# Optimization experiments

Hardware: AMD Instinct MI355X
Metric: run time of the kernel (lower is better)

## Reference

```python
import jax, jax.numpy as jnp
import numpy as np

B, D, N = 65536, 512, 1024  # batch, latent_dim, som_dim**2


def setup_inputs() -> dict:
    key = jax.random.key(0)
    k1, k2, k3, k4, k5 = jax.random.split(key, 5)
    return {
        "x": jax.random.normal(k1, (B, D), dtype=jnp.float32),
        "W": jax.random.normal(k2, (D, D), dtype=jnp.float32) * 0.02,
        "b": jax.random.normal(k3, (D,), dtype=jnp.float32) * 0.02,
        "prototypes": jax.random.normal(k4, (N, D), dtype=jnp.float32),
        "temp_raw": jnp.array([0.5], dtype=jnp.float32),
    }


def reference(x, W, b, prototypes, temp_raw):
    # encoder_fc: Linear(latent_dim, latent_dim)
    z = x @ W.T + b  # [B, D]
    # torch.cdist (p=2) via ||z||^2 + ||p||^2 - 2 z.p, avoids [B,N,D] intermediate
    z_sq = jnp.sum(z * z, axis=-1, keepdims=True)          # [B, 1]
    p_sq = jnp.sum(prototypes * prototypes, axis=-1)        # [N]
    d2 = jnp.maximum(z_sq + p_sq - 2.0 * (z @ prototypes.T), 1e-12)
    dists = jnp.sqrt(d2)                                    # [B, N]
    # temperature = sigmoid(temp_raw) * (1 - 0.001) + 0.001
    temp = jax.nn.sigmoid(temp_raw[0]) * (1.0 - 0.001) + 0.001
    weights = jax.nn.softmax(-dists / temp, axis=-1)        # [B, N]
    blended = weights @ prototypes                          # [B, D]
    return blended, weights
```

## Files before the change

kernel.cpp:

```cpp
#include <hip/hip_runtime.h>

#define DDIM 512
#define NPROT 1024

typedef float fvec4 __attribute__((ext_vector_type(4)));
typedef __bf16 bf16x8 __attribute__((ext_vector_type(8)));
typedef unsigned short us4 __attribute__((ext_vector_type(4)));
typedef unsigned short us8 __attribute__((ext_vector_type(8)));
typedef __attribute__((address_space(1))) unsigned int gu32;
typedef __attribute__((address_space(3))) unsigned int lu32;

__device__ __forceinline__ unsigned short f2bf(float f) {
  unsigned u = __float_as_uint(f);
  u += 0x7fffu + ((u >> 16) & 1u);
  return (unsigned short)(u >> 16);
}
__device__ __forceinline__ float bf2f(unsigned short h) {
  return __uint_as_float(((unsigned)h) << 16);
}
__device__ __forceinline__ void gl_lds16(const void* g, void* l) {
  __builtin_amdgcn_global_load_lds((gu32*)(unsigned long long)g,
                                   (lu32*)(unsigned)(unsigned long long)l,
                                   16, 0, 0);
}

__global__ __launch_bounds__(256) void prep_kernel(
    const float* __restrict__ W, const float* __restrict__ P,
    unsigned short* __restrict__ Wb, unsigned short* __restrict__ Pb,
    unsigned short* __restrict__ PTb, float* __restrict__ psq) {
  __shared__ float tile[32][33];
  const int b = blockIdx.x;
  const int t = threadIdx.x;
  if (b < 256) {
    int e = (b * 256 + t) * 4;
    fvec4 v = *(const fvec4*)(W + e);
    us4 o; o.x = f2bf(v.x); o.y = f2bf(v.y); o.z = f2bf(v.z); o.w = f2bf(v.w);
    *(us4*)(Wb + e) = o;
  } else if (b < 768) {
    int e = ((b - 256) * 256 + t) * 4;
    fvec4 v = *(const fvec4*)(P + e);
    us4 o; o.x = f2bf(v.x); o.y = f2bf(v.y); o.z = f2bf(v.z); o.w = f2bf(v.w);
    *(us4*)(Pb + e) = o;
  } else if (b < 1280) {
    int rel = b - 768;
    int d0 = (rel >> 5) * 32;
    int n0 = (rel & 31) * 32;
    int r = t >> 3;
    int c4 = (t & 7) * 4;
    fvec4 v = *(const fvec4*)(P + (size_t)(n0 + r) * DDIM + d0 + c4);
    tile[r][c4 + 0] = v.x; tile[r][c4 + 1] = v.y;
    tile[r][c4 + 2] = v.z; tile[r][c4 + 3] = v.w;
    __syncthreads();
    us4 o;
    o.x = f2bf(tile[c4 + 0][r]);
    o.y = f2bf(tile[c4 + 1][r]);
    o.z = f2bf(tile[c4 + 2][r]);
    o.w = f2bf(tile[c4 + 3][r]);
    *(us4*)(PTb + (size_t)(d0 + r) * NPROT + n0 + c4) = o;
  } else {
    int l = t & 63;
    int row = (b - 1280) * 4 + (t >> 6);
    const float* pr = P + (size_t)row * DDIM;
    fvec4 a = *(const fvec4*)(pr + l * 4);
    fvec4 c = *(const fvec4*)(pr + 256 + l * 4);
    float s = a.x * a.x + a.y * a.y + a.z * a.z + a.w * a.w +
              c.x * c.x + c.y * c.y + c.z * c.z + c.w * c.w;
    for (int o = 32; o > 0; o >>= 1) s += __shfl_xor(s, o);
    if (l == 0) psq[row] = s;
  }
}

__global__ __launch_bounds__(256) void g1_kernel(
    const float* __restrict__ x, const unsigned short* __restrict__ Wb,
    const float* __restrict__ bias, unsigned short* __restrict__ z) {
  __shared__ unsigned short Ab[128 * 32];
  __shared__ unsigned short Bb[128 * 32];
  const int t = threadIdx.x;
  const int bi = blockIdx.x;
  const int bm = bi >> 2, bn = bi & 3;
  const int w = t >> 6, l = t & 63, lr = l & 15, lq = l >> 4;
  const int wm = (w >> 1) * 64, wn = (w & 1) * 64;
  fvec4 acc[4][4];
#pragma unroll
  for (int r = 0; r < 4; r++)
#pragma unroll
    for (int c = 0; c < 4; c++) acc[r][c] = 0.0f;
  const float* Ag = x + (size_t)bm * 128 * DDIM;
  const unsigned short* Bg = Wb + (size_t)bn * 128 * DDIM;
  for (int k0 = 0; k0 < DDIM; k0 += 32) {
    __syncthreads();
#pragma unroll
    for (int i = 0; i < 2; i++) {
      int c = i * 256 + t;
      gl_lds16(Bg + (size_t)(c >> 2) * DDIM + k0 + (c & 3) * 8, Bb + c * 8);
    }
#pragma unroll
    for (int i = 0; i < 4; i++) {
      int c = i * 256 + t;
      int row = c >> 3, j = (c & 7) * 4;
      fvec4 v = *(const fvec4*)(Ag + (size_t)row * DDIM + k0 + j);
      us4 o; o.x = f2bf(v.x); o.y = f2bf(v.y); o.z = f2bf(v.z); o.w = f2bf(v.w);
      *(us4*)(Ab + row * 32 + j) = o;
    }
    __syncthreads();
    bf16x8 af[4], bfr[4];
#pragma unroll
    for (int r = 0; r < 4; r++)
      af[r] = *(const bf16x8*)(Ab + (wm + r * 16 + lr) * 32 + lq * 8);
#pragma unroll
    for (int c = 0; c < 4; c++)
      bfr[c] = *(const bf16x8*)(Bb + (wn + c * 16 + lr) * 32 + lq * 8);
#pragma unroll
    for (int r = 0; r < 4; r++)
#pragma unroll
      for (int c = 0; c < 4; c++)
        acc[r][c] = __builtin_amdgcn_mfma_f32_16x16x32_bf16(af[r], bfr[c], acc[r][c], 0, 0, 0);
  }
  const int rbase = bm * 128 + wm + lq * 4;
  const int cbase = bn * 128 + wn + lr;
#pragma unroll
  for (int c = 0; c < 4; c++) {
    int col = cbase + c * 16;
    float bc = bias[col];
#pragma unroll
    for (int r = 0; r < 4; r++) {
      int row = rbase + r * 16;
#pragma unroll
      for (int v = 0; v < 4; v++)
        z[(size_t)(row + v) * DDIM + col] = f2bf(acc[r][c][v] + bc);
    }
  }
}

__global__ __launch_bounds__(256) void zsq_kernel(
    const unsigned short* __restrict__ z, float* __restrict__ zsq) {
  const int t = threadIdx.x, l = t & 63;
  const size_t row = (size_t)blockIdx.x * 4 + (t >> 6);
  us8 u = *(const us8*)(z + row * DDIM + l * 8);
  float s = 0.f;
#pragma unroll
  for (int i = 0; i < 8; i++) { float f = bf2f(u[i]); s += f * f; }
  for (int o = 32; o > 0; o >>= 1) s += __shfl_xor(s, o);
  if (l == 0) zsq[row] = s;
}

__global__ __launch_bounds__(256) void g2_kernel(
    const unsigned short* __restrict__ z, const unsigned short* __restrict__ Pb,
    const float* __restrict__ zsq, const float* __restrict__ psq,
    const float* __restrict__ temp_raw, float* __restrict__ logits) {
  __shared__ unsigned short Ab[128 * 32];
  __shared__ unsigned short Bb[128 * 32];
  const int t = threadIdx.x;
  const int bi = blockIdx.x;
  const int bm = bi >> 3, bn = bi & 7;
  const int w = t >> 6, l = t & 63, lr = l & 15, lq = l >> 4;
  const int wm = (w >> 1) * 64, wn = (w & 1) * 64;
  fvec4 acc[4][4];
#pragma unroll
  for (int r = 0; r < 4; r++)
#pragma unroll
    for (int c = 0; c < 4; c++) acc[r][c] = 0.0f;
  const unsigned short* Ag = z + (size_t)bm * 128 * DDIM;
  const unsigned short* Bg = Pb + (size_t)bn * 128 * DDIM;
  for (int k0 = 0; k0 < DDIM; k0 += 32) {
    __syncthreads();
#pragma unroll
    for (int i = 0; i < 2; i++) {
      int c = i * 256 + t;
      gl_lds16(Ag + (size_t)(c >> 2) * DDIM + k0 + (c & 3) * 8, Ab + c * 8);
      gl_lds16(Bg + (size_t)(c >> 2) * DDIM + k0 + (c & 3) * 8, Bb + c * 8);
    }
    __syncthreads();
    bf16x8 af[4], bfr[4];
#pragma unroll
    for (int r = 0; r < 4; r++)
      af[r] = *(const bf16x8*)(Ab + (wm + r * 16 + lr) * 32 + lq * 8);
#pragma unroll
    for (int c = 0; c < 4; c++)
      bfr[c] = *(const bf16x8*)(Bb + (wn + c * 16 + lr) * 32 + lq * 8);
#pragma unroll
    for (int r = 0; r < 4; r++)
#pragma unroll
      for (int c = 0; c < 4; c++)
        acc[r][c] = __builtin_amdgcn_mfma_f32_16x16x32_bf16(af[r], bfr[c], acc[r][c], 0, 0, 0);
  }
  const float temp = 0.999f / (1.0f + __expf(-temp_raw[0])) + 0.001f;
  const float nit = -1.0f / temp;
  const int rbase = bm * 128 + wm + lq * 4;
  const int cbase = bn * 128 + wn + lr;
  float zr[4][4];
#pragma unroll
  for (int r = 0; r < 4; r++)
#pragma unroll
    for (int v = 0; v < 4; v++) zr[r][v] = zsq[rbase + r * 16 + v];
#pragma unroll
  for (int c = 0; c < 4; c++) {
    int col = cbase + c * 16;
    float pc = psq[col];
#pragma unroll
    for (int r = 0; r < 4; r++)
#pragma unroll
      for (int v = 0; v < 4; v++) {
        float d2 = fmaxf(zr[r][v] + pc - 2.0f * acc[r][c][v], 1e-12f);
        logits[(size_t)(rbase + r * 16 + v) * NPROT + col] = nit * sqrtf(d2);
      }
  }
}

__global__ __launch_bounds__(256) void softmax_kernel(float* __restrict__ wio) {
  const int t = threadIdx.x, l = t & 63;
  float* p = wio + ((size_t)blockIdx.x * 4 + (t >> 6)) * NPROT;
  fvec4 v[4];
#pragma unroll
  for (int j = 0; j < 4; j++) v[j] = *(const fvec4*)(p + (j * 64 + l) * 4);
  float m = -3.4e38f;
#pragma unroll
  for (int j = 0; j < 4; j++)
    m = fmaxf(m, fmaxf(fmaxf(v[j].x, v[j].y), fmaxf(v[j].z, v[j].w)));
  for (int o = 32; o > 0; o >>= 1) m = fmaxf(m, __shfl_xor(m, o));
  float s = 0.f;
#pragma unroll
  for (int j = 0; j < 4; j++) {
    v[j].x = __expf(v[j].x - m); v[j].y = __expf(v[j].y - m);
    v[j].z = __expf(v[j].z - m); v[j].w = __expf(v[j].w - m);
    s += v[j].x + v[j].y + v[j].z + v[j].w;
  }
  for (int o = 32; o > 0; o >>= 1) s += __shfl_xor(s, o);
  const float rinv = 1.0f / s;
#pragma unroll
  for (int j = 0; j < 4; j++) {
    v[j] *= rinv;
    *(fvec4*)(p + (j * 64 + l) * 4) = v[j];
  }
}

__global__ __launch_bounds__(512) void g3_kernel(
    const float* __restrict__ wgt, const unsigned short* __restrict__ PTb,
    float* __restrict__ blended) {
  __shared__ unsigned short Ab[128 * 32];
  __shared__ unsigned short Bb[512 * 32];
  const int t = threadIdx.x;
  const int bm = blockIdx.x;
  const int w = t >> 6, l = t & 63, lr = l & 15, lq = l >> 4;
  const int wm = (w >> 2) * 64;
  const int wn = (w & 3) * 128;
  fvec4 acc[4][8];
#pragma unroll
  for (int r = 0; r < 4; r++)
#pragma unroll
    for (int c = 0; c < 8; c++) acc[r][c] = 0.0f;
  const float* Ag = wgt + (size_t)bm * 128 * NPROT;
  for (int k0 = 0; k0 < NPROT; k0 += 32) {
    __syncthreads();
#pragma unroll
    for (int i = 0; i < 4; i++) {
      int c = i * 512 + t;
      gl_lds16(PTb + (size_t)(c >> 2) * NPROT + k0 + (c & 3) * 8, Bb + c * 8);
    }
    {
      int row = t >> 2, j = (t & 3) * 8;
      const float* src = Ag + (size_t)row * NPROT + k0 + j;
      fvec4 v0 = *(const fvec4*)(src);
      fvec4 v1 = *(const fvec4*)(src + 4);
      us8 o;
      o[0] = f2bf(v0.x); o[1] = f2bf(v0.y); o[2] = f2bf(v0.z); o[3] = f2bf(v0.w);
      o[4] = f2bf(v1.x); o[5] = f2bf(v1.y); o[6] = f2bf(v1.z); o[7] = f2bf(v1.w);
      *(us8*)(Ab + row * 32 + j) = o;
    }
    __syncthreads();
    bf16x8 af[4], bfr[8];
#pragma unroll
    for (int r = 0; r < 4; r++)
      af[r] = *(const bf16x8*)(Ab + (wm + r * 16 + lr) * 32 + lq * 8);
#pragma unroll
    for (int c = 0; c < 8; c++)
      bfr[c] = *(const bf16x8*)(Bb + (wn + c * 16 + lr) * 32 + lq * 8);
#pragma unroll
    for (int r = 0; r < 4; r++)
#pragma unroll
      for (int c = 0; c < 8; c++)
        acc[r][c] = __builtin_amdgcn_mfma_f32_16x16x32_bf16(af[r], bfr[c], acc[r][c], 0, 0, 0);
  }
  const int rbase = bm * 128 + wm + lq * 4;
#pragma unroll
  for (int c = 0; c < 8; c++) {
    int col = wn + c * 16 + lr;
#pragma unroll
    for (int r = 0; r < 4; r++) {
      int row = rbase + r * 16;
#pragma unroll
      for (int v = 0; v < 4; v++)
        blended[(size_t)(row + v) * DDIM + col] = acc[r][c][v];
    }
  }
}

extern "C" void kernel_launch(void* const* d_in, const int* in_sizes, int n_in,
                              void* d_out, int out_size, void* d_ws, size_t ws_size,
                              hipStream_t stream) {
  (void)in_sizes; (void)n_in; (void)out_size; (void)ws_size;
  const float* x  = (const float*)d_in[0];
  const float* W  = (const float*)d_in[1];
  const float* bv = (const float*)d_in[2];
  const float* P  = (const float*)d_in[3];
  const float* tr = (const float*)d_in[4];

  float* out = (float*)d_out;
  float* blended = out;
  float* weights = out + (size_t)65536 * DDIM;
  unsigned short* zbuf = (unsigned short*)d_out;

  char* ws = (char*)d_ws;
  unsigned short* Wb  = (unsigned short*)(ws + 0);
  unsigned short* Pb  = (unsigned short*)(ws + 524288);
  unsigned short* PTb = (unsigned short*)(ws + 1572864);
  float* psq = (float*)(ws + 2621440);
  float* zsq = (float*)(ws + 2625536);

  prep_kernel<<<dim3(1536), 256, 0, stream>>>(W, P, Wb, Pb, PTb, psq);
  g1_kernel<<<dim3(2048), 256, 0, stream>>>(x, Wb, bv, zbuf);
  zsq_kernel<<<dim3(16384), 256, 0, stream>>>(zbuf, zsq);
  g2_kernel<<<dim3(4096), 256, 0, stream>>>(zbuf, Pb, zsq, psq, tr, weights);
  softmax_kernel<<<dim3(16384), 256, 0, stream>>>(weights);
  g3_kernel<<<dim3(512), 512, 0, stream>>>(weights, PTb, blended);
}
```

Baseline: 908.2 us.

## Fuse zsq into GEMM1 epilogue and softmax into GEMM2/GEMM3 via row-sum atomics

```diff
diff --git a/kernel.cpp b/kernel.cpp
--- a/kernel.cpp
+++ b/kernel.cpp
@@ -27,7 +27,8 @@
 __global__ __launch_bounds__(256) void prep_kernel(
     const float* __restrict__ W, const float* __restrict__ P,
     unsigned short* __restrict__ Wb, unsigned short* __restrict__ Pb,
-    unsigned short* __restrict__ PTb, float* __restrict__ psq) {
+    unsigned short* __restrict__ PTb, float* __restrict__ psq,
+    float* __restrict__ zsq) {
   __shared__ float tile[32][33];
   const int b = blockIdx.x;
   const int t = threadIdx.x;
@@ -57,7 +58,7 @@
     o.z = f2bf(tile[c4 + 2][r]);
     o.w = f2bf(tile[c4 + 3][r]);
     *(us4*)(PTb + (size_t)(d0 + r) * NPROT + n0 + c4) = o;
-  } else {
+  } else if (b < 1536) {
     int l = t & 63;
     int row = (b - 1280) * 4 + (t >> 6);
     const float* pr = P + (size_t)row * DDIM;
@@ -67,12 +68,23 @@
               c.x * c.x + c.y * c.y + c.z * c.z + c.w * c.w;
     for (int o = 32; o > 0; o >>= 1) s += __shfl_xor(s, o);
     if (l == 0) psq[row] = s;
-  }
+  } else {
+    int i = ((b - 1536) * 256 + t) * 4;
+    fvec4 z4 = 0.0f;
+    *(fvec4*)(zsq + i) = z4;
+  }
+}
+
+__global__ __launch_bounds__(256) void zero_rs_kernel(float* __restrict__ rs) {
+  int i = ((int)blockIdx.x * 256 + (int)threadIdx.x) * 4;
+  fvec4 z4 = 0.0f;
+  *(fvec4*)(rs + i) = z4;
 }
 
 __global__ __launch_bounds__(256) void g1_kernel(
     const float* __restrict__ x, const unsigned short* __restrict__ Wb,
-    const float* __restrict__ bias, unsigned short* __restrict__ z) {
+    const float* __restrict__ bias, unsigned short* __restrict__ z,
+    float* __restrict__ zsq) {
   __shared__ unsigned short Ab[128 * 32];
   __shared__ unsigned short Bb[128 * 32];
   const int t = threadIdx.x;
@@ -118,6 +130,11 @@
   }
   const int rbase = bm * 128 + wm + lq * 4;
   const int cbase = bn * 128 + wn + lr;
+  float sum2[4][4];
+#pragma unroll
+  for (int r = 0; r < 4; r++)
+#pragma unroll
+    for (int v = 0; v < 4; v++) sum2[r][v] = 0.f;
 #pragma unroll
   for (int c = 0; c < 4; c++) {
     int col = cbase + c * 16;
@@ -126,28 +143,29 @@
     for (int r = 0; r < 4; r++) {
       int row = rbase + r * 16;
 #pragma unroll
-      for (int v = 0; v < 4; v++)
-        z[(size_t)(row + v) * DDIM + col] = f2bf(acc[r][c][v] + bc);
-    }
-  }
-}
-
-__global__ __launch_bounds__(256) void zsq_kernel(
-    const unsigned short* __restrict__ z, float* __restrict__ zsq) {
-  const int t = threadIdx.x, l = t & 63;
-  const size_t row = (size_t)blockIdx.x * 4 + (t >> 6);
-  us8 u = *(const us8*)(z + row * DDIM + l * 8);
-  float s = 0.f;
-#pragma unroll
-  for (int i = 0; i < 8; i++) { float f = bf2f(u[i]); s += f * f; }
-  for (int o = 32; o > 0; o >>= 1) s += __shfl_xor(s, o);
-  if (l == 0) zsq[row] = s;
+      for (int v = 0; v < 4; v++) {
+        float zv = acc[r][c][v] + bc;
+        z[(size_t)(row + v) * DDIM + col] = f2bf(zv);
+        sum2[r][v] += zv * zv;
+      }
+    }
+  }
+#pragma unroll
+  for (int r = 0; r < 4; r++)
+#pragma unroll
+    for (int v = 0; v < 4; v++) {
+      float s = sum2[r][v];
+      s += __shfl_xor(s, 1); s += __shfl_xor(s, 2);
+      s += __shfl_xor(s, 4); s += __shfl_xor(s, 8);
+      if (lr == 0) atomicAdd(&zsq[rbase + r * 16 + v], s);
+    }
 }
 
 __global__ __launch_bounds__(256) void g2_kernel(
     const unsigned short* __restrict__ z, const unsigned short* __restrict__ Pb,
     const float* __restrict__ zsq, const float* __restrict__ psq,
-    const float* __restrict__ temp_raw, float* __restrict__ logits) {
+    const float* __restrict__ temp_raw, float* __restrict__ ewgt,
+    float* __restrict__ rowsum) {
   __shared__ unsigned short Ab[128 * 32];
   __shared__ unsigned short Bb[128 * 32];
   const int t = threadIdx.x;
@@ -193,6 +211,11 @@
   for (int r = 0; r < 4; r++)
 #pragma unroll
     for (int v = 0; v < 4; v++) zr[r][v] = zsq[rbase + r * 16 + v];
+  float esum[4][4];
+#pragma unroll
+  for (int r = 0; r < 4; r++)
+#pragma unroll
+    for (int v = 0; v < 4; v++) esum[r][v] = 0.f;
 #pragma unroll
   for (int c = 0; c < 4; c++) {
     int col = cbase + c * 16;
@@ -202,41 +225,25 @@
 #pragma unroll
       for (int v = 0; v < 4; v++) {
         float d2 = fmaxf(zr[r][v] + pc - 2.0f * acc[r][c][v], 1e-12f);
-        logits[(size_t)(rbase + r * 16 + v) * NPROT + col] = nit * sqrtf(d2);
+        float e = __expf(nit * sqrtf(d2));
+        ewgt[(size_t)(rbase + r * 16 + v) * NPROT + col] = e;
+        esum[r][v] += e;
       }
   }
-}
-
-__global__ __launch_bounds__(256) void softmax_kernel(float* __restrict__ wio) {
-  const int t = threadIdx.x, l = t & 63;
-  float* p = wio + ((size_t)blockIdx.x * 4 + (t >> 6)) * NPROT;
-  fvec4 v[4];
-#pragma unroll
-  for (int j = 0; j < 4; j++) v[j] = *(const fvec4*)(p + (j * 64 + l) * 4);
-  float m = -3.4e38f;
-#pragma unroll
-  for (int j = 0; j < 4; j++)
-    m = fmaxf(m, fmaxf(fmaxf(v[j].x, v[j].y), fmaxf(v[j].z, v[j].w)));
-  for (int o = 32; o > 0; o >>= 1) m = fmaxf(m, __shfl_xor(m, o));
-  float s = 0.f;
-#pragma unroll
-  for (int j = 0; j < 4; j++) {
-    v[j].x = __expf(v[j].x - m); v[j].y = __expf(v[j].y - m);
-    v[j].z = __expf(v[j].z - m); v[j].w = __expf(v[j].w - m);
-    s += v[j].x + v[j].y + v[j].z + v[j].w;
-  }
-  for (int o = 32; o > 0; o >>= 1) s += __shfl_xor(s, o);
-  const float rinv = 1.0f / s;
-#pragma unroll
-  for (int j = 0; j < 4; j++) {
-    v[j] *= rinv;
-    *(fvec4*)(p + (j * 64 + l) * 4) = v[j];
-  }
+#pragma unroll
+  for (int r = 0; r < 4; r++)
+#pragma unroll
+    for (int v = 0; v < 4; v++) {
+      float s = esum[r][v];
+      s += __shfl_xor(s, 1); s += __shfl_xor(s, 2);
+      s += __shfl_xor(s, 4); s += __shfl_xor(s, 8);
+      if (lr == 0) atomicAdd(&rowsum[rbase + r * 16 + v], s);
+    }
 }
 
 __global__ __launch_bounds__(512) void g3_kernel(
-    const float* __restrict__ wgt, const unsigned short* __restrict__ PTb,
-    float* __restrict__ blended) {
+    float* __restrict__ wgt, const unsigned short* __restrict__ PTb,
+    const float* __restrict__ rowsum, float* __restrict__ blended) {
   __shared__ unsigned short Ab[128 * 32];
   __shared__ unsigned short Bb[512 * 32];
   const int t = threadIdx.x;
@@ -249,7 +256,10 @@
   for (int r = 0; r < 4; r++)
 #pragma unroll
     for (int c = 0; c < 8; c++) acc[r][c] = 0.0f;
-  const float* Ag = wgt + (size_t)bm * 128 * NPROT;
+  const int arow = t >> 2;
+  const int aj = (t & 3) * 8;
+  float* Arow = wgt + (size_t)(bm * 128 + arow) * NPROT + aj;
+  const float rinv = 1.0f / rowsum[bm * 128 + arow];
   for (int k0 = 0; k0 < NPROT; k0 += 32) {
     __syncthreads();
 #pragma unroll
@@ -258,14 +268,16 @@
       gl_lds16(PTb + (size_t)(c >> 2) * NPROT + k0 + (c & 3) * 8, Bb + c * 8);
     }
     {
-      int row = t >> 2, j = (t & 3) * 8;
-      const float* src = Ag + (size_t)row * NPROT + k0 + j;
-      fvec4 v0 = *(const fvec4*)(src);
+      float* src = Arow + k0;
+      fvec4 v0 = *(const fvec4*)src;
       fvec4 v1 = *(const fvec4*)(src + 4);
+      v0 *= rinv; v1 *= rinv;
+      *(fvec4*)src = v0;
+      *(fvec4*)(src + 4) = v1;
       us8 o;
       o[0] = f2bf(v0.x); o[1] = f2bf(v0.y); o[2] = f2bf(v0.z); o[3] = f2bf(v0.w);
       o[4] = f2bf(v1.x); o[5] = f2bf(v1.y); o[6] = f2bf(v1.z); o[7] = f2bf(v1.w);
-      *(us8*)(Ab + row * 32 + j) = o;
+      *(us8*)(Ab + arow * 32 + aj) = o;
     }
     __syncthreads();
     bf16x8 af[4], bfr[8];
@@ -316,11 +328,11 @@
   unsigned short* PTb = (unsigned short*)(ws + 1572864);
   float* psq = (float*)(ws + 2621440);
   float* zsq = (float*)(ws + 2625536);
-
-  prep_kernel<<<dim3(1536), 256, 0, stream>>>(W, P, Wb, Pb, PTb, psq);
-  g1_kernel<<<dim3(2048), 256, 0, stream>>>(x, Wb, bv, zbuf);
-  zsq_kernel<<<dim3(16384), 256, 0, stream>>>(zbuf, zsq);
-  g2_kernel<<<dim3(4096), 256, 0, stream>>>(zbuf, Pb, zsq, psq, tr, weights);
-  softmax_kernel<<<dim3(16384), 256, 0, stream>>>(weights);
-  g3_kernel<<<dim3(512), 512, 0, stream>>>(weights, PTb, blended);
-}
+  float* rowsum = (float*)(ws + 0);
+
+  prep_kernel<<<dim3(1600), 256, 0, stream>>>(W, P, Wb, Pb, PTb, psq, zsq);
+  g1_kernel<<<dim3(2048), 256, 0, stream>>>(x, Wb, bv, zbuf, zsq);
+  zero_rs_kernel<<<dim3(64), 256, 0, stream>>>(rowsum);
+  g2_kernel<<<dim3(4096), 256, 0, stream>>>(zbuf, Pb, zsq, psq, tr, weights, rowsum);
+  g3_kernel<<<dim3(512), 512, 0, stream>>>(weights, PTb, rowsum, blended);
+}
```

Result: faster. 881.3 us (-3.0%).
